# Optimization experiments

Measured on AMD Instinct MI355X. Metric: run time of the kernel, lower is better.

The kernel has to match this reference:

```python
import jax, jax.numpy as jnp
import numpy as np

D_MODEL = 1024
H = 16
D_K = D_MODEL // H
D_FF = 4096
EPS = 1e-6
NEG = -1e9


def layer_norm(x, alpha, beta):
    # Custom LN: scalar alpha/beta, unbiased std, eps added to std (not var)
    mean = jnp.mean(x, axis=-1, keepdims=True)
    std = jnp.std(x, axis=-1, ddof=1, keepdims=True)
    return alpha * (x - mean) / (std + EPS) + beta


def setup_inputs() -> dict:
    key = jax.random.key(0)
    ks = jax.random.split(key, 16)
    B, S = 4, 2048
    s = 1.0 / np.sqrt(D_MODEL)
    inp = {
        "x": jax.random.normal(ks[0], (B, S, D_MODEL), dtype=jnp.float32),
        "src_mask": jax.random.randint(ks[1], (B, 1, 1, S), 0, 2, dtype=jnp.int32),
        "wq": jax.random.normal(ks[2], (D_MODEL, D_MODEL), jnp.float32) * s,
        "bq": jnp.zeros((D_MODEL,), jnp.float32),
        "wk": jax.random.normal(ks[3], (D_MODEL, D_MODEL), jnp.float32) * s,
        "bk": jnp.zeros((D_MODEL,), jnp.float32),
        "wv": jax.random.normal(ks[4], (D_MODEL, D_MODEL), jnp.float32) * s,
        "bv": jnp.zeros((D_MODEL,), jnp.float32),
        "wo": jax.random.normal(ks[5], (D_MODEL, D_MODEL), jnp.float32) * s,
        "bo": jnp.zeros((D_MODEL,), jnp.float32),
        "w1": jax.random.normal(ks[6], (D_MODEL, D_FF), jnp.float32) * s,
        "b1": jnp.zeros((D_FF,), jnp.float32),
        "w2": jax.random.normal(ks[7], (D_FF, D_MODEL), jnp.float32) * (1.0 / np.sqrt(D_FF)),
        "b2": jnp.zeros((D_MODEL,), jnp.float32),
        "a1": jnp.ones((1,), jnp.float32),
        "be1": jnp.zeros((1,), jnp.float32),
        "a2": jnp.ones((1,), jnp.float32),
        "be2": jnp.zeros((1,), jnp.float32),
    }
    return inp


def reference(x, src_mask, wq, bq, wk, bk, wv, bv, wo, bo, w1, b1, w2, b2, a1, be1, a2, be2):
    B, S, _ = x.shape

    # --- residual 1: self-attention on pre-LN input (dropout = identity, eval) ---
    xn = layer_norm(x, a1, be1)
    q = (xn @ wq + bq).reshape(B, S, H, D_K).transpose(0, 2, 1, 3)  # [B,H,S,Dk]
    k = (xn @ wk + bk).reshape(B, S, H, D_K).transpose(0, 2, 1, 3)
    v = (xn @ wv + bv).reshape(B, S, H, D_K).transpose(0, 2, 1, 3)

    scores = jnp.einsum("bhqd,bhkd->bhqk", q, k) / jnp.sqrt(jnp.float32(D_K))
    scores = jnp.where(src_mask == 0, jnp.float32(NEG), scores)
    attn = jax.nn.softmax(scores, axis=-1)
    ctx = jnp.einsum("bhqk,bhkd->bhqd", attn, v)  # [B,H,S,Dk]
    ctx = ctx.transpose(0, 2, 1, 3).reshape(B, S, D_MODEL)
    attn_out = ctx @ wo + bo
    x = x + attn_out

    # --- residual 2: feed-forward on pre-LN input ---
    xn2 = layer_norm(x, a2, be2)
    ff = jax.nn.relu(xn2 @ w1 + b1) @ w2 + b2
    return x + ff
```

## Files before the change

### kernel.cpp

```cpp
#include <hip/hip_runtime.h>
#include <stdint.h>

typedef unsigned short u16;
typedef __attribute__((ext_vector_type(8))) short short8;
typedef __attribute__((ext_vector_type(4))) float f32x4;
typedef __attribute__((ext_vector_type(4))) u16 u16x4;
typedef __attribute__((ext_vector_type(4))) uint32_t u32x4;

#define NB 4
#define SEQ 2048
#define DM 1024
#define NH 16
#define DKh 64
#define DFF 4096
#define LOG2E 1.44269504089f

__device__ __forceinline__ u16 f2bf(float f) {
  union { float f; uint32_t u; } v; v.f = f;
  uint32_t u = v.u;
  return (u16)((u + 0x7FFFu + ((u >> 16) & 1u)) >> 16);
}

__device__ __forceinline__ uint32_t cvtpk(float lo, float hi) {
  uint32_t r;
  asm("v_cvt_pk_bf16_f32 %0, %1, %2" : "=v"(r) : "v"(lo), "v"(hi));
  return r;
}

__device__ __forceinline__ float fexp2(float x) {
  float r;
  asm("v_exp_f32 %0, %1" : "=v"(r) : "v"(x));
  return r;
}

__device__ __forceinline__ void gl16(const u16* g, u16* l) {
  __builtin_amdgcn_global_load_lds((const __attribute__((address_space(1))) void*)g,
                                   (__attribute__((address_space(3))) void*)l, 16, 0, 0);
}

__global__ __launch_bounds__(256) void transpose_bf16(const float* __restrict__ src,
                                                      u16* __restrict__ dst, int R, int C) {
  __shared__ float tile[32][33];
  int tx = threadIdx.x, ty = threadIdx.y;
  int c0 = blockIdx.x * 32, r0 = blockIdx.y * 32;
#pragma unroll
  for (int i = 0; i < 32; i += 8)
    tile[ty + i][tx] = src[(size_t)(r0 + ty + i) * C + c0 + tx];
  __syncthreads();
#pragma unroll
  for (int i = 0; i < 32; i += 8)
    dst[(size_t)(c0 + ty + i) * R + r0 + tx] = f2bf(tile[tx][ty + i]);
}

__global__ __launch_bounds__(256) void bias_cat(const float* __restrict__ bq,
                                                const float* __restrict__ bk,
                                                const float* __restrict__ bv,
                                                float* __restrict__ o) {
  int i = blockIdx.x * 256 + threadIdx.x;
  if (i < 3072) o[i] = (i < 1024) ? bq[i] : ((i < 2048) ? bk[i - 1024] : bv[i - 2048]);
}

__global__ __launch_bounds__(256) void mask_bias(const int* __restrict__ m,
                                                 float* __restrict__ o) {
  int i = blockIdx.x * 256 + threadIdx.x;
  o[i] = m[i] ? 0.0f : -1e9f;
}

__global__ __launch_bounds__(256) void ln_bf16(const float* __restrict__ x,
                                               u16* __restrict__ out,
                                               const float* __restrict__ alpha,
                                               const float* __restrict__ beta) {
  int row = blockIdx.x;
  const float4* xr = (const float4*)(x + (size_t)row * DM);
  int t = threadIdx.x;
  float4 v = xr[t];
  float s = v.x + v.y + v.z + v.w;
  float s2 = v.x * v.x + v.y * v.y + v.z * v.z + v.w * v.w;
#pragma unroll
  for (int m = 1; m < 64; m <<= 1) { s += __shfl_xor(s, m); s2 += __shfl_xor(s2, m); }
  __shared__ float red[8];
  int wid = t >> 6, lane = t & 63;
  if (lane == 0) { red[wid] = s; red[wid + 4] = s2; }
  __syncthreads();
  float S = red[0] + red[1] + red[2] + red[3];
  float S2 = red[4] + red[5] + red[6] + red[7];
  float mean = S * (1.0f / DM);
  float var = fmaxf((S2 - S * mean) * (1.0f / (DM - 1)), 0.0f);
  float inv = alpha[0] / (sqrtf(var) + 1e-6f);
  float bet = beta[0];
  u16x4 o;
  o[0] = f2bf((v.x - mean) * inv + bet);
  o[1] = f2bf((v.y - mean) * inv + bet);
  o[2] = f2bf((v.z - mean) * inv + bet);
  o[3] = f2bf((v.w - mean) * inv + bet);
  *(u16x4*)(out + (size_t)row * DM + t * 4) = o;
}

template <int MODE>
__global__ __launch_bounds__(512, 1) void gemm256(const u16* __restrict__ A,
                                                  const u16* __restrict__ WT,
                                                  const float* __restrict__ bias,
                                                  u16* __restrict__ outp,
                                                  int M, int N, int K, float qscale) {
  extern __shared__ u16 lds[];
  int tid = threadIdx.x;
  int lane = tid & 63, wid = tid >> 6;
  int lr = lane & 15, lg = lane >> 4;
  int wr = wid >> 2, wc = wid & 3;
  int nbx = N >> 8;
  int nwg = (M >> 8) * nbx;
  int lid = blockIdx.x;
  int swz = (lid & 7) * (nwg >> 3) + (lid >> 3);
  int m0 = (swz / nbx) << 8, n0 = (swz % nbx) << 8;

  int rowih = wid * 16 + (lane >> 2);
  int cchunk = lane & 3;
  int csrc = cchunk ^ ((rowih >> 1) & 3);
  size_t a_src = (size_t)(m0 + rowih) * K + csrc * 8;
  size_t b_src = (size_t)(n0 + rowih) * K + csrc * 8;
  u16* a_dst = lds + rowih * 32 + cchunk * 8;
  u16* b_dst = a_dst + 8192;

#define STAGE_A(B_, T_) do { \
    const u16* s_ = A + a_src + (size_t)(T_) * 32; \
    gl16(s_, a_dst + (B_) * 16384); \
    gl16(s_ + (size_t)128 * K, a_dst + (B_) * 16384 + 4096); \
  } while (0)
#define STAGE_B(B_, T_) do { \
    const u16* s_ = WT + b_src + (size_t)(T_) * 32; \
    gl16(s_, b_dst + (B_) * 16384); \
    gl16(s_ + (size_t)128 * K, b_dst + (B_) * 16384 + 4096); \
  } while (0)

  int rchunk = (lg ^ ((lr >> 1) & 3)) * 8;
  int offA[8], offB[4];
#pragma unroll
  for (int i = 0; i < 8; ++i) offA[i] = (wr * 128 + i * 16 + lr) * 32 + rchunk;
#pragma unroll
  for (int j = 0; j < 4; ++j) offB[j] = (wc * 64 + j * 16 + lr) * 32 + rchunk;

  f32x4 acc[8][4] = {};

  int NT = K >> 5;
  STAGE_A(0, 0); STAGE_B(0, 0);
  STAGE_A(1, 1); STAGE_B(1, 1);
  asm volatile("s_waitcnt vmcnt(4)" ::: "memory");
  __builtin_amdgcn_s_barrier();

  int buf = 0;
  for (int t = 0; t < NT; ++t) {
    const u16* la = lds + buf * 16384;
    const u16* lb = la + 8192;
    int b2 = buf - 1; if (b2 < 0) b2 += 3;
    short8 af0[4], bfr[4];
#pragma unroll
    for (int i = 0; i < 4; ++i) af0[i] = *(const short8*)&la[offA[i]];
#pragma unroll
    for (int j = 0; j < 4; ++j) bfr[j] = *(const short8*)&lb[offB[j]];
    if (t + 2 < NT) STAGE_A(b2, t + 2);
    __builtin_amdgcn_s_setprio(1);
#pragma unroll
    for (int i = 0; i < 4; ++i)
#pragma unroll
      for (int j = 0; j < 4; ++j)
        acc[i][j] = __builtin_amdgcn_mfma_f32_16x16x32_bf16(af0[i], bfr[j], acc[i][j], 0, 0, 0);
    __builtin_amdgcn_s_setprio(0);
    short8 af1[4];
#pragma unroll
    for (int i = 0; i < 4; ++i) af1[i] = *(const short8*)&la[offA[i + 4]];
    if (t + 2 < NT) STAGE_B(b2, t + 2);
    if (t < NT - 2) asm volatile("s_waitcnt vmcnt(4)" ::: "memory");
    else            asm volatile("s_waitcnt vmcnt(0)" ::: "memory");
    __builtin_amdgcn_s_setprio(1);
#pragma unroll
    for (int i = 0; i < 4; ++i)
#pragma unroll
      for (int j = 0; j < 4; ++j)
        acc[i + 4][j] = __builtin_amdgcn_mfma_f32_16x16x32_bf16(af1[i], bfr[j], acc[i + 4][j], 0, 0, 0);
    __builtin_amdgcn_s_setprio(0);
    __builtin_amdgcn_s_barrier();
    __builtin_amdgcn_sched_barrier(0);
    buf = (buf == 2) ? 0 : buf + 1;
  }
#undef STAGE_A
#undef STAGE_B

#pragma unroll
  for (int i = 0; i < 8; ++i) {
#pragma unroll
    for (int j = 0; j < 4; ++j) {
      int col = n0 + wc * 64 + j * 16 + lr;
      float bi = bias[col];
      int rbase = m0 + wr * 128 + i * 16 + lg * 4;
      if (MODE == 0) {
        int which = col >> 10, nc = col & 1023;
        int hh = nc >> 6, dd = nc & 63;
        int bb = rbase >> 11, ss = rbase & 2047;
        if (which == 2) {
          u16* vtb = outp + (size_t)2 * (8u << 20);
          u16x4 pk;
#pragma unroll
          for (int r = 0; r < 4; ++r) pk[r] = f2bf(acc[i][j][r] + bi);
          *(u16x4*)&vtb[((size_t)(bb * NH + hh) * DKh + dd) * SEQ + ss] = pk;
        } else {
          u16* dst = outp + (size_t)which * (8u << 20);
          float sc = (which == 0) ? qscale : 1.0f;
#pragma unroll
          for (int r = 0; r < 4; ++r)
            dst[((size_t)(bb * NH + hh) * SEQ + (ss + r)) * DKh + dd] = f2bf((acc[i][j][r] + bi) * sc);
        }
      } else {
#pragma unroll
        for (int r = 0; r < 4; ++r)
          outp[(size_t)(rbase + r) * N + col] = f2bf(fmaxf(acc[i][j][r] + bi, 0.0f));
      }
    }
  }
}

__global__ __launch_bounds__(512, 4) void gemm_v2(const u16* __restrict__ A,
                                                  const u16* __restrict__ WT,
                                                  const float* __restrict__ bias,
                                                  const float* __restrict__ resid,
                                                  float* __restrict__ outp,
                                                  int M, int N, int K) {
  extern __shared__ u16 lds[];
  int tid = threadIdx.x;
  int lane = tid & 63, wid = tid >> 6;
  int lr = lane & 15, lg = lane >> 4;
  int wr = wid >> 1, wc = wid & 1;
  int nbx = N >> 7;
  int nwg = (M >> 8) * nbx;
  int lid = blockIdx.x;
  int swz = (lid & 7) * (nwg >> 3) + (lid >> 3);
  int m0 = (swz / nbx) << 8, n0 = (swz % nbx) << 7;

  int sr = tid >> 2;
  int sch = tid & 3;
  int scs = sch ^ ((sr >> 1) & 3);
  size_t a_src = (size_t)(m0 + sr) * K + scs * 8;
  size_t b_src = (size_t)(n0 + sr) * K + scs * 8;
  u16* a_dst = lds + sr * 32 + sch * 8;
  u16* b_dst = lds + 8192 + sr * 32 + sch * 8;

#define STAGE(B_, T_) do { \
    gl16(A + a_src + (size_t)(T_) * 32, a_dst + (B_) * 12288); \
    gl16(A + a_src + (size_t)128 * K + (size_t)(T_) * 32, a_dst + (B_) * 12288 + 4096); \
    gl16(WT + b_src + (size_t)(T_) * 32, b_dst + (B_) * 12288); \
  } while (0)

  int rchunk = (lg ^ ((lr >> 1) & 3)) * 8;
  int offA[4], offB[4];
#pragma unroll
  for (int i = 0; i < 4; ++i) offA[i] = (wr * 64 + i * 16 + lr) * 32 + rchunk;
#pragma unroll
  for (int j = 0; j < 4; ++j) offB[j] = 8192 + (wc * 64 + j * 16 + lr) * 32 + rchunk;

  f32x4 acc[4][4] = {};

  int NT = K >> 5;
  STAGE(0, 0);
  STAGE(1, 1);
  asm volatile("s_waitcnt vmcnt(3)" ::: "memory");
  __builtin_amdgcn_s_barrier();

  int buf = 0;
  for (int t = 0; t < NT; ++t) {
    const u16* la = lds + buf * 12288;
    int b2 = buf - 1; if (b2 < 0) b2 += 3;
    short8 af[4], bfr[4];
#pragma unroll
    for (int i = 0; i < 4; ++i) af[i] = *(const short8*)&la[offA[i]];
#pragma unroll
    for (int j = 0; j < 4; ++j) bfr[j] = *(const short8*)&la[offB[j]];
    if (t + 2 < NT) STAGE(b2, t + 2);
    __builtin_amdgcn_s_setprio(1);
#pragma unroll
    for (int i = 0; i < 4; ++i)
#pragma unroll
      for (int j = 0; j < 4; ++j)
        acc[i][j] = __builtin_amdgcn_mfma_f32_16x16x32_bf16(af[i], bfr[j], acc[i][j], 0, 0, 0);
    __builtin_amdgcn_s_setprio(0);
    if (t < NT - 2) asm volatile("s_waitcnt vmcnt(3)" ::: "memory");
    else            asm volatile("s_waitcnt vmcnt(0)" ::: "memory");
    __builtin_amdgcn_s_barrier();
    __builtin_amdgcn_sched_barrier(0);
    buf = (buf == 2) ? 0 : buf + 1;
  }
#undef STAGE

#pragma unroll
  for (int i = 0; i < 4; ++i) {
#pragma unroll
    for (int j = 0; j < 4; ++j) {
      int col = n0 + wc * 64 + j * 16 + lr;
      float bi = bias[col];
      int rbase = m0 + wr * 64 + i * 16 + lg * 4;
#pragma unroll
      for (int r = 0; r < 4; ++r) {
        size_t idx = (size_t)(rbase + r) * N + col;
        outp[idx] = resid[idx] + acc[i][j][r] + bi;
      }
    }
  }
}

__global__ __launch_bounds__(256) void attn_fwd(const u16* __restrict__ q,
                                                const u16* __restrict__ k,
                                                const u16* __restrict__ vt,
                                                const float* __restrict__ fbb,
                                                u16* __restrict__ ctx) {
  __shared__ u16 Ks[64 * 64];
  __shared__ u16 Vs[64 * 64];
  int tid = threadIdx.x;
  int wid = tid >> 6, lane = tid & 63;
  int lr = lane & 15, lg = lane >> 4;
  int bh = blockIdx.y;
  int b = bh >> 4, hh = bh & 15;
  int q0 = blockIdx.x * 128;
  const u16* qbase = q + (size_t)bh * SEQ * DKh;
  const u16* kbase = k + (size_t)bh * SEQ * DKh;
  const u16* vbase = vt + (size_t)bh * DKh * SEQ;
  const float* fbbase = fbb + b * SEQ;

  short8 qf[2][2];
#pragma unroll
  for (int i = 0; i < 2; ++i)
#pragma unroll
    for (int kk = 0; kk < 2; ++kk)
      qf[i][kk] = *(const short8*)(qbase + (size_t)(q0 + wid * 32 + i * 16 + lr) * DKh + kk * 32 + lg * 8);

  int sr = tid >> 3;
  int scg = (tid & 7) * 8;
  int kwix[2];
#pragma unroll
  for (int it = 0; it < 2; ++it) {
    int r = it * 32 + sr;
    kwix[it] = r * 64 + (scg ^ ((r & 7) << 3));
  }
  int jsrc = scg >> 4;
  int pos1 = (jsrc & 1) * 32 + ((scg & 15) >> 2) * 8 + (jsrc >> 1) * 4;
  int vwix[2][2];
#pragma unroll
  for (int it = 0; it < 2; ++it) {
    int r = it * 32 + sr;
    int sw = (r & 7) << 3;
    vwix[it][0] = r * 64 + (pos1 ^ sw);
    vwix[it][1] = r * 64 + ((pos1 + 8) ^ sw);
  }
  int swzc = (lr & 7) << 3;

  short8 ka[2], va[2];
#pragma unroll
  for (int it = 0; it < 2; ++it) {
    int r = it * 32 + sr;
    ka[it] = *(const short8*)(kbase + (size_t)r * DKh + scg);
    va[it] = *(const short8*)(vbase + (size_t)r * SEQ + scg);
  }

  f32x4 ot[2][4] = {};
  float mrow[2] = {-3e38f, -3e38f};
  float lsum[2] = {0.0f, 0.0f};

  for (int kv0 = 0; kv0 < SEQ; kv0 += 64) {
    __syncthreads();
#pragma unroll
    for (int it = 0; it < 2; ++it) {
      *(short8*)&Ks[kwix[it]] = ka[it];
      u16x4 vlo, vhi;
#pragma unroll
      for (int e = 0; e < 4; ++e) { vlo[e] = ((u16*)&va[it])[e]; vhi[e] = ((u16*)&va[it])[e + 4]; }
      *(u16x4*)&Vs[vwix[it][0]] = vlo;
      *(u16x4*)&Vs[vwix[it][1]] = vhi;
    }
    if (kv0 + 64 < SEQ) {
      int nv = kv0 + 64;
#pragma unroll
      for (int it = 0; it < 2; ++it) {
        int r = it * 32 + sr;
        ka[it] = *(const short8*)(kbase + (size_t)(nv + r) * DKh + scg);
        va[it] = *(const short8*)(vbase + (size_t)r * SEQ + nv + scg);
      }
    }
    __syncthreads();

    f32x4 st[2][4] = {};
    __builtin_amdgcn_s_setprio(1);
#pragma unroll
    for (int kk = 0; kk < 2; ++kk) {
      short8 kf[4];
#pragma unroll
      for (int j = 0; j < 4; ++j)
        kf[j] = *(const short8*)&Ks[(j * 16 + lr) * 64 + ((kk * 32 + lg * 8) ^ swzc)];
#pragma unroll
      for (int i = 0; i < 2; ++i)
#pragma unroll
        for (int j = 0; j < 4; ++j)
          st[i][j] = __builtin_amdgcn_mfma_f32_16x16x32_bf16(kf[j], qf[i][kk], st[i][j], 0, 0, 0);
    }
    __builtin_amdgcn_s_setprio(0);

    float fb[4][4];
#pragma unroll
    for (int j = 0; j < 4; ++j) {
      float4 f4 = *(const float4*)(fbbase + kv0 + j * 16 + lg * 4);
      fb[j][0] = f4.x; fb[j][1] = f4.y; fb[j][2] = f4.z; fb[j][3] = f4.w;
    }

    u32x4 pa[2][2];
#pragma unroll
    for (int i = 0; i < 2; ++i) {
      float p[4][4];
      float mx = -3e38f;
#pragma unroll
      for (int j = 0; j < 4; ++j)
#pragma unroll
        for (int r = 0; r < 4; ++r) {
          float s = st[i][j][r] + fb[j][r];
          p[j][r] = s;
          mx = fmaxf(mx, s);
        }
      mx = fmaxf(mx, __shfl_xor(mx, 16));
      mx = fmaxf(mx, __shfl_xor(mx, 32));
      float mnew = fmaxf(mrow[i], mx);
      if (!__all(mnew - mrow[i] <= 8.0f)) {
        float corr = fexp2(mrow[i] - mnew);
        lsum[i] *= corr;
#pragma unroll
        for (int jd = 0; jd < 4; ++jd)
#pragma unroll
          for (int r = 0; r < 4; ++r) ot[i][jd][r] *= corr;
        mrow[i] = mnew;
      }
      float ps = 0.0f;
#pragma unroll
      for (int j = 0; j < 4; ++j)
#pragma unroll
        for (int r = 0; r < 4; ++r) {
          float pv = fexp2(p[j][r] - mrow[i]);
          p[j][r] = pv;
          ps += pv;
        }
      ps += __shfl_xor(ps, 16);
      ps += __shfl_xor(ps, 32);
      lsum[i] += ps;
#pragma unroll
      for (int ks = 0; ks < 2; ++ks) {
        pa[i][ks][0] = cvtpk(p[ks][0], p[ks][1]);
        pa[i][ks][1] = cvtpk(p[ks][2], p[ks][3]);
        pa[i][ks][2] = cvtpk(p[ks + 2][0], p[ks + 2][1]);
        pa[i][ks][3] = cvtpk(p[ks + 2][2], p[ks + 2][3]);
      }
    }

    __builtin_amdgcn_s_setprio(1);
#pragma unroll
    for (int ks = 0; ks < 2; ++ks) {
      short8 vf[4];
#pragma unroll
      for (int jd = 0; jd < 4; ++jd)
        vf[jd] = *(const short8*)&Vs[(jd * 16 + lr) * 64 + ((ks * 32 + lg * 8) ^ swzc)];
#pragma unroll
      for (int i = 0; i < 2; ++i)
#pragma unroll
        for (int jd = 0; jd < 4; ++jd)
          ot[i][jd] = __builtin_amdgcn_mfma_f32_16x16x32_bf16(vf[jd], *(short8*)&pa[i][ks], ot[i][jd], 0, 0, 0);
    }
    __builtin_amdgcn_s_setprio(0);
  }

  float inv0 = 1.0f / lsum[0], inv1 = 1.0f / lsum[1];
  __syncthreads();
  u16* ep = (wid < 2) ? (Ks + wid * 2048) : (Vs + (wid - 2) * 2048);
#pragma unroll
  for (int i = 0; i < 2; ++i) {
    float inv = i ? inv1 : inv0;
#pragma unroll
    for (int jd = 0; jd < 4; ++jd) {
      uint32_t w0 = cvtpk(ot[i][jd][0] * inv, ot[i][jd][1] * inv);
      uint32_t w1 = cvtpk(ot[i][jd][2] * inv, ot[i][jd][3] * inv);
      uint32_t pk2[2] = {w0, w1};
      *(u16x4*)&ep[(i * 16 + lr) * 64 + ((jd * 16 + lg * 4) ^ swzc)] = *(u16x4*)pk2;
    }
  }
  __syncthreads();
  int q_ = lane >> 1;
  size_t orow = ((size_t)b * SEQ + q0 + wid * 32 + q_) * DM + hh * DKh;
#pragma unroll
  for (int it = 0; it < 4; ++it) {
    int dc = (lane & 1) * 32 + it * 8;
    short8 vv = *(const short8*)&ep[q_ * 64 + (dc ^ ((q_ & 7) << 3))];
    *(short8*)(ctx + orow + dc) = vv;
  }
}

extern "C" void kernel_launch(void* const* d_in, const int* in_sizes, int n_in,
                              void* d_out, int out_size, void* d_ws, size_t ws_size,
                              hipStream_t stream) {
  const float* x   = (const float*)d_in[0];
  const int*   msk = (const int*)d_in[1];
  const float* wq  = (const float*)d_in[2];
  const float* bq  = (const float*)d_in[3];
  const float* wk  = (const float*)d_in[4];
  const float* bk  = (const float*)d_in[5];
  const float* wv  = (const float*)d_in[6];
  const float* bv  = (const float*)d_in[7];
  const float* wo  = (const float*)d_in[8];
  const float* bo  = (const float*)d_in[9];
  const float* w1  = (const float*)d_in[10];
  const float* b1  = (const float*)d_in[11];
  const float* w2  = (const float*)d_in[12];
  const float* b2  = (const float*)d_in[13];
  const float* a1  = (const float*)d_in[14];
  const float* be1 = (const float*)d_in[15];
  const float* a2  = (const float*)d_in[16];
  const float* be2 = (const float*)d_in[17];
  float* out = (float*)d_out;

  u16* wqT = (u16*)d_ws;
  u16* wkT = wqT + (1u << 20);
  u16* wvT = wkT + (1u << 20);
  u16* woT = wvT + (1u << 20);
  u16* w1T = woT + (1u << 20);
  u16* w2T = w1T + (4u << 20);
  u16* xn  = w2T + (4u << 20);
  u16* qb  = xn  + (8u << 20);
  u16* kb  = qb  + (8u << 20);
  u16* vtb = kb  + (8u << 20);
  u16* ctx = vtb + (8u << 20);
  u16* hb  = qb;
  float* bcat = (float*)ctx;
  float* fbb  = (float*)(ctx + (8u << 20));

  (void)hipFuncSetAttribute((const void*)gemm256<0>, hipFuncAttributeMaxDynamicSharedMemorySize, 96 * 1024);
  (void)hipFuncSetAttribute((const void*)gemm256<3>, hipFuncAttributeMaxDynamicSharedMemorySize, 96 * 1024);
  (void)hipFuncSetAttribute((const void*)gemm_v2, hipFuncAttributeMaxDynamicSharedMemorySize, 72 * 1024);

  dim3 tb(32, 8);
  transpose_bf16<<<dim3(32, 32), tb, 0, stream>>>(wq, wqT, DM, DM);
  transpose_bf16<<<dim3(32, 32), tb, 0, stream>>>(wk, wkT, DM, DM);
  transpose_bf16<<<dim3(32, 32), tb, 0, stream>>>(wv, wvT, DM, DM);
  transpose_bf16<<<dim3(32, 32), tb, 0, stream>>>(wo, woT, DM, DM);
  transpose_bf16<<<dim3(128, 32), tb, 0, stream>>>(w1, w1T, DM, DFF);
  transpose_bf16<<<dim3(32, 128), tb, 0, stream>>>(w2, w2T, DFF, DM);
  bias_cat<<<12, 256, 0, stream>>>(bq, bk, bv, bcat);
  mask_bias<<<32, 256, 0, stream>>>(msk, fbb);

  ln_bf16<<<NB * SEQ, 256, 0, stream>>>(x, xn, a1, be1);

  gemm256<0><<<384, 512, 96 * 1024, stream>>>(xn, wqT, bcat, qb, NB * SEQ, 3 * DM, DM, 0.125f * LOG2E);

  attn_fwd<<<dim3(SEQ / 128, NB * NH), 256, 0, stream>>>(qb, kb, vtb, fbb, ctx);

  gemm_v2<<<256, 512, 72 * 1024, stream>>>(ctx, woT, bo, x, out, NB * SEQ, DM, DM);

  ln_bf16<<<NB * SEQ, 256, 0, stream>>>(out, xn, a2, be2);

  gemm256<3><<<512, 512, 96 * 1024, stream>>>(xn, w1T, b1, hb, NB * SEQ, DFF, DM, 1.0f);

  gemm_v2<<<256, 512, 72 * 1024, stream>>>(hb, w2T, b2, out, out, NB * SEQ, DM, DFF);
}
```

Baseline: 422.9 us.

## Compact unmasked key positions so attention skips masked keys

```diff
diff --git a/kernel.cpp b/kernel.cpp
--- a/kernel.cpp
+++ b/kernel.cpp
@@ -60,10 +60,68 @@
   if (i < 3072) o[i] = (i < 1024) ? bq[i] : ((i < 2048) ? bk[i - 1024] : bv[i - 2048]);
 }
 
-__global__ __launch_bounds__(256) void mask_bias(const int* __restrict__ m,
-                                                 float* __restrict__ o) {
-  int i = blockIdx.x * 256 + threadIdx.x;
-  o[i] = m[i] ? 0.0f : -1e9f;
+__global__ __launch_bounds__(1024) void compact_idx(const int* __restrict__ msk,
+                                                    int* __restrict__ cidx,
+                                                    int* __restrict__ lArr,
+                                                    int* __restrict__ lpArr,
+                                                    float* __restrict__ fbbc) {
+  int b = blockIdx.x;
+  int t = threadIdx.x;
+  int lane = t & 63, w = t >> 6;
+  int i0 = t * 2, i1 = t * 2 + 1;
+  int m0 = msk[b * SEQ + i0] ? 1 : 0;
+  int m1 = msk[b * SEQ + i1] ? 1 : 0;
+  int s = m0 + m1;
+  int run = s;
+#pragma unroll
+  for (int d = 1; d < 64; d <<= 1) {
+    int v = __shfl_up(run, d);
+    if (lane >= d) run += v;
+  }
+  __shared__ int wtot[16];
+  __shared__ int woff[17];
+  if (lane == 63) wtot[w] = run;
+  __syncthreads();
+  if (t == 0) {
+    int acc = 0;
+#pragma unroll
+    for (int i = 0; i < 16; ++i) { woff[i] = acc; acc += wtot[i]; }
+    woff[16] = acc;
+  }
+  __syncthreads();
+  int excl = run - s + woff[w];
+  if (m0) cidx[b * SEQ + excl] = i0;
+  if (m1) cidx[b * SEQ + excl + m0] = i1;
+  int L = woff[16];
+  int LP = (L + 63) & ~63;
+  if (LP == 0) LP = 64;
+  if (t == 0) { lArr[b] = L; lpArr[b] = LP; }
+  for (int l = t; l < SEQ; l += 1024) {
+    if (l >= L) cidx[b * SEQ + l] = 0;
+    fbbc[b * SEQ + l] = (l < L) ? 0.0f : -1e9f;
+  }
+}
+
+__global__ __launch_bounds__(256) void gather_vt(const u16* __restrict__ vtb,
+                                                 const int* __restrict__ cidx,
+                                                 const int* __restrict__ lpArr,
+                                                 u16* __restrict__ vthat) {
+  int d = blockIdx.x;
+  int bh = blockIdx.y;
+  int b = bh >> 4;
+  int t = threadIdx.x;
+  __shared__ u16 row[SEQ];
+  const u16* src = vtb + ((size_t)bh * DKh + d) * SEQ;
+  *(short8*)&row[t * 8] = *(const short8*)(src + t * 8);
+  __syncthreads();
+  int LP = lpArr[b];
+  u16* dst = vthat + ((size_t)bh * DKh + d) * SEQ;
+  const int* ib = cidx + b * SEQ;
+  for (int l2 = t; l2 * 2 < LP; l2 += 256) {
+    uint32_t lo = row[ib[l2 * 2]];
+    uint32_t hi = row[ib[l2 * 2 + 1]];
+    *(uint32_t*)&dst[l2 * 2] = lo | (hi << 16);
+  }
 }
 
 __global__ __launch_bounds__(256) void ln_bf16(const float* __restrict__ x,
@@ -308,7 +366,10 @@
 __global__ __launch_bounds__(256) void attn_fwd(const u16* __restrict__ q,
                                                 const u16* __restrict__ k,
                                                 const u16* __restrict__ vt,
-                                                const float* __restrict__ fbb,
+                                                const int* __restrict__ cidx,
+                                                const int* __restrict__ lArr,
+                                                const int* __restrict__ lpArr,
+                                                const float* __restrict__ fbbc,
                                                 u16* __restrict__ ctx) {
   __shared__ u16 Ks[64 * 64];
   __shared__ u16 Vs[64 * 64];
@@ -321,7 +382,10 @@
   const u16* qbase = q + (size_t)bh * SEQ * DKh;
   const u16* kbase = k + (size_t)bh * SEQ * DKh;
   const u16* vbase = vt + (size_t)bh * DKh * SEQ;
-  const float* fbbase = fbb + b * SEQ;
+  const float* fbbase = fbbc + b * SEQ;
+  const int* ib = cidx + b * SEQ;
+  int Lb = lArr[b];
+  int LP = lpArr[b];
 
   short8 qf[2][2];
 #pragma unroll
@@ -351,18 +415,19 @@
   int swzc = (lr & 7) << 3;
 
   short8 ka[2], va[2];
-#pragma unroll
-  for (int it = 0; it < 2; ++it) {
-    int r = it * 32 + sr;
-    ka[it] = *(const short8*)(kbase + (size_t)r * DKh + scg);
-    va[it] = *(const short8*)(vbase + (size_t)r * SEQ + scg);
+  {
+    int id0 = ib[sr], id1 = ib[32 + sr];
+    ka[0] = *(const short8*)(kbase + (size_t)id0 * DKh + scg);
+    ka[1] = *(const short8*)(kbase + (size_t)id1 * DKh + scg);
+    va[0] = *(const short8*)(vbase + (size_t)sr * SEQ + scg);
+    va[1] = *(const short8*)(vbase + (size_t)(32 + sr) * SEQ + scg);
   }
 
   f32x4 ot[2][4] = {};
   float mrow[2] = {-3e38f, -3e38f};
   float lsum[2] = {0.0f, 0.0f};
 
-  for (int kv0 = 0; kv0 < SEQ; kv0 += 64) {
+  for (int kv0 = 0; kv0 < LP; kv0 += 64) {
     __syncthreads();
 #pragma unroll
     for (int it = 0; it < 2; ++it) {
@@ -373,14 +438,13 @@
       *(u16x4*)&Vs[vwix[it][0]] = vlo;
       *(u16x4*)&Vs[vwix[it][1]] = vhi;
     }
-    if (kv0 + 64 < SEQ) {
+    if (kv0 + 64 < LP) {
       int nv = kv0 + 64;
-#pragma unroll
-      for (int it = 0; it < 2; ++it) {
-        int r = it * 32 + sr;
-        ka[it] = *(const short8*)(kbase + (size_t)(nv + r) * DKh + scg);
-        va[it] = *(const short8*)(vbase + (size_t)r * SEQ + nv + scg);
-      }
+      int id0 = ib[nv + sr], id1 = ib[nv + 32 + sr];
+      ka[0] = *(const short8*)(kbase + (size_t)id0 * DKh + scg);
+      ka[1] = *(const short8*)(kbase + (size_t)id1 * DKh + scg);
+      va[0] = *(const short8*)(vbase + (size_t)sr * SEQ + nv + scg);
+      va[1] = *(const short8*)(vbase + (size_t)(32 + sr) * SEQ + nv + scg);
     }
     __syncthreads();
 
@@ -400,26 +464,32 @@
     }
     __builtin_amdgcn_s_setprio(0);
 
-    float fb[4][4];
-#pragma unroll
-    for (int j = 0; j < 4; ++j) {
-      float4 f4 = *(const float4*)(fbbase + kv0 + j * 16 + lg * 4);
-      fb[j][0] = f4.x; fb[j][1] = f4.y; fb[j][2] = f4.z; fb[j][3] = f4.w;
-    }
+    bool tail = (kv0 + 64 > Lb);
 
     u32x4 pa[2][2];
 #pragma unroll
     for (int i = 0; i < 2; ++i) {
       float p[4][4];
+      if (tail) {
+#pragma unroll
+        for (int j = 0; j < 4; ++j) {
+          float4 f4 = *(const float4*)(fbbase + kv0 + j * 16 + lg * 4);
+          p[j][0] = st[i][j][0] + f4.x;
+          p[j][1] = st[i][j][1] + f4.y;
+          p[j][2] = st[i][j][2] + f4.z;
+          p[j][3] = st[i][j][3] + f4.w;
+        }
+      } else {
+#pragma unroll
+        for (int j = 0; j < 4; ++j)
+#pragma unroll
+          for (int r = 0; r < 4; ++r) p[j][r] = st[i][j][r];
+      }
       float mx = -3e38f;
 #pragma unroll
       for (int j = 0; j < 4; ++j)
 #pragma unroll
-        for (int r = 0; r < 4; ++r) {
-          float s = st[i][j][r] + fb[j][r];
-          p[j][r] = s;
-          mx = fmaxf(mx, s);
-        }
+        for (int r = 0; r < 4; ++r) mx = fmaxf(mx, p[j][r]);
       mx = fmaxf(mx, __shfl_xor(mx, 16));
       mx = fmaxf(mx, __shfl_xor(mx, 32));
       float mnew = fmaxf(mrow[i], mx);
@@ -530,7 +600,10 @@
   u16* ctx = vtb + (8u << 20);
   u16* hb  = qb;
   float* bcat = (float*)ctx;
-  float* fbb  = (float*)(ctx + (8u << 20));
+  int*   cidx = (int*)(ctx + (8u << 20));
+  int*   lArr = cidx + NB * SEQ;
+  int*   lpArr = lArr + 16;
+  float* fbbc = (float*)(lpArr + 16);
 
   (void)hipFuncSetAttribute((const void*)gemm256<0>, hipFuncAttributeMaxDynamicSharedMemorySize, 96 * 1024);
   (void)hipFuncSetAttribute((const void*)gemm256<3>, hipFuncAttributeMaxDynamicSharedMemorySize, 96 * 1024);
@@ -544,13 +617,15 @@
   transpose_bf16<<<dim3(128, 32), tb, 0, stream>>>(w1, w1T, DM, DFF);
   transpose_bf16<<<dim3(32, 128), tb, 0, stream>>>(w2, w2T, DFF, DM);
   bias_cat<<<12, 256, 0, stream>>>(bq, bk, bv, bcat);
-  mask_bias<<<32, 256, 0, stream>>>(msk, fbb);
+  compact_idx<<<NB, 1024, 0, stream>>>(msk, cidx, lArr, lpArr, fbbc);
 
   ln_bf16<<<NB * SEQ, 256, 0, stream>>>(x, xn, a1, be1);
 
   gemm256<0><<<384, 512, 96 * 1024, stream>>>(xn, wqT, bcat, qb, NB * SEQ, 3 * DM, DM, 0.125f * LOG2E);
 
-  attn_fwd<<<dim3(SEQ / 128, NB * NH), 256, 0, stream>>>(qb, kb, vtb, fbb, ctx);
+  gather_vt<<<dim3(DKh, NB * NH), 256, 0, stream>>>(vtb, cidx, lpArr, xn);
+
+  attn_fwd<<<dim3(SEQ / 128, NB * NH), 256, 0, stream>>>(qb, kb, xn, cidx, lArr, lpArr, fbbc, ctx);
 
   gemm_v2<<<256, 512, 72 * 1024, stream>>>(ctx, woT, bo, x, out, NB * SEQ, DM, DM);
 
```

Measured after the change: 376.3 us. 1.12x faster.
